# Optimization experiments

Measured on AMD Instinct MI355X. Metric: run time of the kernel, lower is better.

## Reference

```python
import jax, jax.numpy as jnp
import numpy as np

TOP_K = 8
N_EXPERTS = 64
AUX_ALPHA = 0.1


def setup_inputs() -> dict:
    key = jax.random.key(0)
    k1, k2 = jax.random.split(key)
    hidden_states = jax.random.normal(k1, (4, 4096, 2048), dtype=jnp.float32)
    # kaiming_uniform_(a=sqrt(5)) -> U(-bound, bound), bound = sqrt(6/((1+5)*fan_in)) = 1/sqrt(fan_in)
    bound = 1.0 / np.sqrt(2048.0)
    weight = jax.random.uniform(k2, (N_EXPERTS, 2048), dtype=jnp.float32, minval=-bound, maxval=bound)
    return {"hidden_states": hidden_states, "weight": weight}


def reference(hidden_states, weight):
    bsz, seq_len, h = hidden_states.shape
    x = hidden_states.reshape(-1, h)                      # [N, H], N = bsz*seq_len
    logits = jnp.einsum('nh,eh->ne', x, weight)           # [N, E]
    scores = jax.nn.softmax(logits, axis=-1)              # [N, E]
    topk_weight, topk_idx = jax.lax.top_k(scores, TOP_K)  # [N, k]
    # normalize top-k probs
    topk_weight = topk_weight / (topk_weight.sum(axis=-1, keepdims=True) + 1e-20)
    # seq-aux load-balancing loss (training path, seq_aux=True)
    idx_b = topk_idx.reshape(bsz, seq_len * TOP_K)        # [B, S*k]
    ce = jnp.zeros((bsz, N_EXPERTS), dtype=jnp.float32)
    ce = jax.vmap(lambda c, i: c.at[i].add(1.0))(ce, idx_b)
    ce = ce / (seq_len * TOP_K / N_EXPERTS)
    scores_seq_mean = scores.reshape(bsz, seq_len, N_EXPERTS).mean(axis=1)  # [B, E]
    aux_loss = ((ce * scores_seq_mean).sum(axis=1)).mean() * AUX_ALPHA
    return topk_idx, topk_weight, aux_loss
```

## Files before the change

kernel.cpp:

```cpp
#include <hip/hip_runtime.h>
#include <math.h>

#define N_TOK 16384
#define HDIM 2048
#define NE 64
#define TOPK 8
#define NB 4
#define SEQ 4096
#define TT 64
#define HC 64
#define LSTR 68
#define SSTR 65

__global__ __launch_bounds__(256) void moe_gate_main(
    const float* __restrict__ x, const float* __restrict__ w,
    float* __restrict__ out_idx, float* __restrict__ out_w,
    float* __restrict__ ws_ce, float* __restrict__ ws_ssum)
{
    __shared__ float xs[TT][LSTR];
    __shared__ float wl[NE][LSTR];
    __shared__ float sc[TT][SSTR];
    __shared__ unsigned ce_loc[NE];
    __shared__ float sred[4][NE];

    const int tid = threadIdx.x;
    const int blk = blockIdx.x;
    const int t0  = blk * TT;
    const int tx  = tid & 15;
    const int ty  = tid >> 4;

    if (tid < NE) ce_loc[tid] = 0u;

    float4 acc[4][4];
    #pragma unroll
    for (int i = 0; i < 4; ++i)
        #pragma unroll
        for (int j = 0; j < 4; ++j) acc[i][j] = make_float4(0.f, 0.f, 0.f, 0.f);

    float4 xr[4], wr[4];
    #pragma unroll
    for (int r = 0; r < 4; ++r) {
        int f = tid + r * 256;
        int row = f >> 4, h4 = f & 15;
        xr[r] = *(const float4*)&x[(long)(t0 + row) * HDIM + (h4 << 2)];
        wr[r] = *(const float4*)&w[(long)row * HDIM + (h4 << 2)];
    }

    const int qord[16] = {3,2,1,0, 7,6,5,4, 11,10,9,8, 15,14,13,12};

    for (int hc = 0; hc < HDIM; hc += HC) {
        #pragma unroll
        for (int r = 0; r < 4; ++r) {
            int f = tid + r * 256;
            int row = f >> 4, h4 = f & 15;
            *(float4*)&xs[row][h4 << 2] = xr[r];
            *(float4*)&wl[row][h4 << 2] = wr[r];
        }
        __syncthreads();
        if (hc + HC < HDIM) {
            #pragma unroll
            for (int r = 0; r < 4; ++r) {
                int f = tid + r * 256;
                int row = f >> 4, h4 = f & 15;
                xr[r] = *(const float4*)&x[(long)(t0 + row) * HDIM + hc + HC + (h4 << 2)];
                wr[r] = *(const float4*)&w[(long)row * HDIM + hc + HC + (h4 << 2)];
            }
        }
        #pragma unroll
        for (int qi = 0; qi < 16; ++qi) {
            const int h4 = qord[qi];
            float4 xv[4], wv[4];
            #pragma unroll
            for (int i = 0; i < 4; ++i) xv[i] = *(const float4*)&xs[ty + 16 * i][h4 << 2];
            #pragma unroll
            for (int j = 0; j < 4; ++j) wv[j] = *(const float4*)&wl[tx + 16 * j][h4 << 2];
            {
                #pragma clang fp contract(off)
                #pragma unroll
                for (int i = 0; i < 4; ++i)
                    #pragma unroll
                    for (int j = 0; j < 4; ++j) {
                        acc[i][j].x = acc[i][j].x + xv[i].x * wv[j].x;
                        acc[i][j].y = acc[i][j].y + xv[i].y * wv[j].y;
                        acc[i][j].z = acc[i][j].z + xv[i].z * wv[j].z;
                        acc[i][j].w = acc[i][j].w + xv[i].w * wv[j].w;
                    }
            }
        }
        __syncthreads();
    }

    #pragma unroll
    for (int i = 0; i < 4; ++i)
        #pragma unroll
        for (int j = 0; j < 4; ++j) {
            float4 a = acc[i][j];
            sc[ty + 16 * i][tx + 16 * j] = (a.x + a.y) + (a.z + a.w);
        }
    __syncthreads();

    const int wid  = tid >> 6;
    const int lane = tid & 63;
    const int b    = blk >> 6;
    float ssum = 0.f;

    for (int r = 0; r < 16; ++r) {
        const int tok = wid * 16 + r;
        const float v = sc[tok][lane];
        float m = v;
        #pragma unroll
        for (int off = 32; off; off >>= 1) m = fmaxf(m, __shfl_xor(m, off));
        const float p = (float)exp((double)(v - m));
        float racc[8];
        #pragma unroll
        for (int a = 0; a < 8; ++a) racc[a] = __shfl(p, a);
        #pragma unroll
        for (int t = 1; t < 8; ++t)
            #pragma unroll
            for (int a = 0; a < 8; ++a) racc[a] = racc[a] + __shfl(p, 8 * t + a);
        const float s = ((racc[0] + racc[1]) + (racc[2] + racc[3]))
                      + ((racc[4] + racc[5]) + (racc[6] + racc[7]));
        const float q = p / s;
        ssum += q;

        unsigned kk = __float_as_uint(q) & ~3u;
        float myw = 0.f; int myi = 0;
        #pragma unroll
        for (int k = 0; k < TOPK; ++k) {
            unsigned bvk = kk; int bi = lane;
            #pragma unroll
            for (int off = 32; off; off >>= 1) {
                unsigned ovk = __shfl_xor(bvk, off);
                int      oi  = __shfl_xor(bi, off);
                if (ovk > bvk || (ovk == bvk && oi < bi)) { bvk = ovk; bi = oi; }
            }
            const float swv = __shfl(q, bi);
            if (lane == k)  { myw = swv; myi = bi; }
            if (lane == bi) kk = 0u;
        }
        float g[8];
        #pragma unroll
        for (int a = 0; a < 8; ++a) g[a] = __shfl(myw, a);
        const float wsum = ((g[0] + g[1]) + (g[2] + g[3]))
                         + ((g[4] + g[5]) + (g[6] + g[7]));

        const long gt = t0 + tok;
        if (lane < TOPK) {
            out_idx[gt * TOPK + lane] = (float)myi;
            out_w [gt * TOPK + lane] = myw / (wsum + 1e-20f);
            atomicAdd(&ce_loc[myi], 1u);
        }
    }

    sred[wid][lane] = ssum;
    __syncthreads();
    if (tid < NE) {
        float t = sred[0][tid] + sred[1][tid] + sred[2][tid] + sred[3][tid];
        atomicAdd(&ws_ssum[b * NE + tid], t);
        atomicAdd(&ws_ce  [b * NE + tid], (float)ce_loc[tid]);
    }
}

__global__ void moe_gate_aux(const float* __restrict__ ws_ce,
                             const float* __restrict__ ws_ssum,
                             float* __restrict__ out_aux)
{
    const int lane = threadIdx.x;
    float part = 0.f;
    #pragma unroll
    for (int b = 0; b < NB; ++b)
        part += ws_ce[b * NE + lane] * ws_ssum[b * NE + lane];
    #pragma unroll
    for (int off = 32; off; off >>= 1) part += __shfl_xor(part, off);
    if (lane == 0)
        out_aux[0] = part * (0.1f / (4.0f * 512.0f * 4096.0f));
}

extern "C" void kernel_launch(void* const* d_in, const int* in_sizes, int n_in,
                              void* d_out, int out_size, void* d_ws, size_t ws_size,
                              hipStream_t stream)
{
    const float* x = (const float*)d_in[0];
    const float* w = (const float*)d_in[1];
    float* out      = (float*)d_out;
    float* out_idx  = out;
    float* out_w    = out + (long)N_TOK * TOPK;
    float* out_aux  = out + 2L * N_TOK * TOPK;
    float* ws_ce    = (float*)d_ws;
    float* ws_ssum  = ws_ce + NB * NE;

    hipMemsetAsync(d_ws, 0, 2 * NB * NE * sizeof(float), stream);
    moe_gate_main<<<N_TOK / TT, 256, 0, stream>>>(x, w, out_idx, out_w, ws_ce, ws_ssum);
    moe_gate_aux<<<1, 64, 0, stream>>>(ws_ce, ws_ssum, out_aux);
}
```

Before: 446.3 us.

## Shrink token tile to 16 per block to launch more workgroups

Reduces the tokens per block from 64 to 16, so the grid grows from 256 to 1024 blocks and each thread computes a 1x4 output tile instead of 4x4. It also adds a min-blocks-per-CU launch bound. The aim is to fill the many CUs on the device, since 256 blocks underuse the GPU. The cost is that the weight matrix is reloaded from global/L2 and into LDS four times as often, with lower arithmetic intensity per LDS load.

```diff
diff --git a/kernel.cpp b/kernel.cpp
--- a/kernel.cpp
+++ b/kernel.cpp
@@ -7,12 +7,12 @@
 #define TOPK 8
 #define NB 4
 #define SEQ 4096
-#define TT 64
+#define TT 16
 #define HC 64
 #define LSTR 68
 #define SSTR 65
 
-__global__ __launch_bounds__(256) void moe_gate_main(
+__global__ __launch_bounds__(256, 4) void moe_gate_main(
     const float* __restrict__ x, const float* __restrict__ w,
     float* __restrict__ out_idx, float* __restrict__ out_w,
     float* __restrict__ ws_ce, float* __restrict__ ws_ssum)
@@ -31,81 +31,81 @@
 
     if (tid < NE) ce_loc[tid] = 0u;
 
-    float4 acc[4][4];
+    float4 acc[4];
     #pragma unroll
-    for (int i = 0; i < 4; ++i)
+    for (int j = 0; j < 4; ++j) acc[j] = make_float4(0.f, 0.f, 0.f, 0.f);
+
+    float4 xr, wr[4];
+    {
+        int row = tid >> 4, h4 = tid & 15;
+        xr = *(const float4*)&x[(long)(t0 + row) * HDIM + (h4 << 2)];
         #pragma unroll
-        for (int j = 0; j < 4; ++j) acc[i][j] = make_float4(0.f, 0.f, 0.f, 0.f);
-
-    float4 xr[4], wr[4];
-    #pragma unroll
-    for (int r = 0; r < 4; ++r) {
-        int f = tid + r * 256;
-        int row = f >> 4, h4 = f & 15;
-        xr[r] = *(const float4*)&x[(long)(t0 + row) * HDIM + (h4 << 2)];
-        wr[r] = *(const float4*)&w[(long)row * HDIM + (h4 << 2)];
+        for (int r = 0; r < 4; ++r) {
+            int f = tid + r * 256;
+            int wrow = f >> 4, wh4 = f & 15;
+            wr[r] = *(const float4*)&w[(long)wrow * HDIM + (wh4 << 2)];
+        }
     }
 
     const int qord[16] = {3,2,1,0, 7,6,5,4, 11,10,9,8, 15,14,13,12};
 
     for (int hc = 0; hc < HDIM; hc += HC) {
-        #pragma unroll
-        for (int r = 0; r < 4; ++r) {
-            int f = tid + r * 256;
-            int row = f >> 4, h4 = f & 15;
-            *(float4*)&xs[row][h4 << 2] = xr[r];
-            *(float4*)&wl[row][h4 << 2] = wr[r];
+        {
+            int row = tid >> 4, h4 = tid & 15;
+            *(float4*)&xs[row][h4 << 2] = xr;
+            #pragma unroll
+            for (int r = 0; r < 4; ++r) {
+                int f = tid + r * 256;
+                int wrow = f >> 4, wh4 = f & 15;
+                *(float4*)&wl[wrow][wh4 << 2] = wr[r];
+            }
         }
         __syncthreads();
         if (hc + HC < HDIM) {
+            int row = tid >> 4, h4 = tid & 15;
+            xr = *(const float4*)&x[(long)(t0 + row) * HDIM + hc + HC + (h4 << 2)];
             #pragma unroll
             for (int r = 0; r < 4; ++r) {
                 int f = tid + r * 256;
-                int row = f >> 4, h4 = f & 15;
-                xr[r] = *(const float4*)&x[(long)(t0 + row) * HDIM + hc + HC + (h4 << 2)];
-                wr[r] = *(const float4*)&w[(long)row * HDIM + hc + HC + (h4 << 2)];
+                int wrow = f >> 4, wh4 = f & 15;
+                wr[r] = *(const float4*)&w[(long)wrow * HDIM + hc + HC + (wh4 << 2)];
             }
         }
         #pragma unroll
         for (int qi = 0; qi < 16; ++qi) {
             const int h4 = qord[qi];
-            float4 xv[4], wv[4];
-            #pragma unroll
-            for (int i = 0; i < 4; ++i) xv[i] = *(const float4*)&xs[ty + 16 * i][h4 << 2];
+            float4 xv = *(const float4*)&xs[ty][h4 << 2];
+            float4 wv[4];
             #pragma unroll
             for (int j = 0; j < 4; ++j) wv[j] = *(const float4*)&wl[tx + 16 * j][h4 << 2];
             {
                 #pragma clang fp contract(off)
                 #pragma unroll
-                for (int i = 0; i < 4; ++i)
-                    #pragma unroll
-                    for (int j = 0; j < 4; ++j) {
-                        acc[i][j].x = acc[i][j].x + xv[i].x * wv[j].x;
-                        acc[i][j].y = acc[i][j].y + xv[i].y * wv[j].y;
-                        acc[i][j].z = acc[i][j].z + xv[i].z * wv[j].z;
-                        acc[i][j].w = acc[i][j].w + xv[i].w * wv[j].w;
-                    }
+                for (int j = 0; j < 4; ++j) {
+                    acc[j].x = acc[j].x + xv.x * wv[j].x;
+                    acc[j].y = acc[j].y + xv.y * wv[j].y;
+                    acc[j].z = acc[j].z + xv.z * wv[j].z;
+                    acc[j].w = acc[j].w + xv.w * wv[j].w;
+                }
             }
         }
         __syncthreads();
     }
 
     #pragma unroll
-    for (int i = 0; i < 4; ++i)
-        #pragma unroll
-        for (int j = 0; j < 4; ++j) {
-            float4 a = acc[i][j];
-            sc[ty + 16 * i][tx + 16 * j] = (a.x + a.y) + (a.z + a.w);
-        }
+    for (int j = 0; j < 4; ++j) {
+        float4 a = acc[j];
+        sc[ty][tx + 16 * j] = (a.x + a.y) + (a.z + a.w);
+    }
     __syncthreads();
 
     const int wid  = tid >> 6;
     const int lane = tid & 63;
-    const int b    = blk >> 6;
+    const int b    = blk >> 8;
     float ssum = 0.f;
 
-    for (int r = 0; r < 16; ++r) {
-        const int tok = wid * 16 + r;
+    for (int r = 0; r < 4; ++r) {
+        const int tok = wid * 4 + r;
         const float v = sc[tok][lane];
         float m = v;
         #pragma unroll
```

After: 450.9 us. Within noise of the previous version (+1.0%).
